# Kernel tuning notes

Measured on AMD Instinct MI355X. Metric: run time of the kernel, lower is better.

Reference implementation:

```python
import jax, jax.numpy as jnp
import numpy as np

V, E, H, T, B, D, L = 32000, 512, 512, 128, 4, 4, 2
C0, C1 = 2000, 10000          # adaptive softmax cutoffs
NT = T - D + 1


def setup_inputs() -> dict:
    key = jax.random.key(0)
    ks = jax.random.split(key, 18)
    s = 0.02
    x = jax.random.randint(ks[0], (B, T), 1, V)
    lengths = jnp.sort(jax.random.randint(ks[1], (B,), D, T + 1))[::-1]
    lengths = lengths.at[0].set(T)
    # graph predictor output: per-layer attention matrices [B, L, T, T]
    G = jax.nn.softmax(jax.random.normal(ks[2], (B, L, T, T)), axis=-1)
    emb = (jax.random.normal(ks[3], (V, E)) * s).at[0].set(0.0)  # padding_idx=0
    enc_w_ih = jax.random.normal(ks[4], (L, 3 * H, H)) * s
    enc_w_hh = jax.random.normal(ks[5], (L, 3 * H, H)) * s
    enc_b_ih = jnp.zeros((L, 3 * H))
    enc_b_hh = jnp.zeros((L, 3 * H))
    dec_w_ih = jax.random.normal(ks[6], (3 * H, E)) * s
    dec_w_hh = jax.random.normal(ks[7], (3 * H, H)) * s
    dec_b_ih = jnp.zeros((3 * H,))
    dec_b_hh = jnp.zeros((3 * H,))
    head_w = jax.random.normal(ks[8], (C0 + 2, H)) * s
    t0_proj = jax.random.normal(ks[9], (H // 4, H)) * s
    t0_out = jax.random.normal(ks[10], (C1 - C0, H // 4)) * s
    t1_proj = jax.random.normal(ks[11], (H // 16, H)) * s
    t1_out = jax.random.normal(ks[12], (V - C1, H // 16)) * s
    return dict(x=x, lengths=lengths, G=G, emb=emb,
                enc_w_ih=enc_w_ih, enc_w_hh=enc_w_hh, enc_b_ih=enc_b_ih, enc_b_hh=enc_b_hh,
                dec_w_ih=dec_w_ih, dec_w_hh=dec_w_hh, dec_b_ih=dec_b_ih, dec_b_hh=dec_b_hh,
                head_w=head_w, t0_proj=t0_proj, t0_out=t0_out, t1_proj=t1_proj, t1_out=t1_out)


def gru_step(xt, h, w_ih, w_hh, b_ih, b_hh):
    """torch nn.GRU/GRUCell math; works on arbitrary leading dims."""
    gi = xt @ w_ih.T + b_ih
    gh = h @ w_hh.T + b_hh
    i_r, i_z, i_n = jnp.split(gi, 3, axis=-1)
    h_r, h_z, h_n = jnp.split(gh, 3, axis=-1)
    r = jax.nn.sigmoid(i_r + h_r)
    z = jax.nn.sigmoid(i_z + h_z)
    n = jnp.tanh(i_n + r * h_n)
    return (1.0 - z) * n + z * h


def adaptive_log_prob(h, head_w, t0_proj, t0_out, t1_proj, t1_out):
    """torch AdaptiveLogSoftmaxWithLoss.log_prob: h [N,H] -> [N,V]."""
    head_lp = jax.nn.log_softmax(h @ head_w.T, axis=-1)                      # [N, C0+2]
    lp0 = head_lp[:, C0:C0 + 1] + jax.nn.log_softmax((h @ t0_proj.T) @ t0_out.T, axis=-1)
    lp1 = head_lp[:, C0 + 1:C0 + 2] + jax.nn.log_softmax((h @ t1_proj.T) @ t1_out.T, axis=-1)
    return jnp.concatenate([head_lp[:, :C0], lp0, lp1], axis=-1)


def reference(x, lengths, G, emb, enc_w_ih, enc_w_hh, enc_b_ih, enc_b_hh,
              dec_w_ih, dec_w_hh, dec_b_ih, dec_b_hh,
              head_w, t0_proj, t0_out, t1_proj, t1_out):
    b = x.shape[0]
    input_f = emb[x]                      # [B,T,E] (dropout p=0)
    embedded = input_f
    # ---- encoder: graph-weighted aggregation + GRUCell per layer ----
    for l in range(enc_w_ih.shape[0]):
        wgt = jnp.einsum('bji,bjd->bid', G[:, l], input_f)   # G_l^T @ input_f
        input_f = gru_step(wgt, input_f, enc_w_ih[l], enc_w_hh[l], enc_b_ih[l], enc_b_hh[l])
    # ---- decoder: length-D GRU window per start position t ----
    t_idx = jnp.arange(NT)
    d_idx = jnp.arange(D)
    tok_idx = jnp.broadcast_to(t_idx[None, :, None] + d_idx[None, None, :] - 1, (b, NT, D))
    tok_idx = tok_idx.at[:, 0, 0].set(lengths - 1)           # t=0,d=0 uses embedded[lengths-1]
    wins = jnp.take_along_axis(embedded, tok_idx.reshape(b, -1)[:, :, None], axis=1)
    wins = wins.reshape(b, NT, D, E)
    h0 = input_f[:, :NT, :]                                  # [B,NT,H]
    def step(h, xd):
        hn = gru_step(xd, h, dec_w_ih, dec_w_hh, dec_b_ih, dec_b_hh)
        return hn, hn
    _, hs = jax.lax.scan(step, h0, jnp.moveaxis(wins, 2, 0))  # [D,B,NT,H]
    hs = jnp.moveaxis(hs, 0, 2)                               # [B,NT,D,H]
    # pad_packed_sequence zeros hidden beyond per-row lens = min(lengths - t, D)
    valid = (t_idx[None, :, None] + d_idx[None, None, :]) < lengths[:, None, None]
    hs = jnp.where(valid[..., None], hs, 0.0)
    lp = adaptive_log_prob(hs.reshape(-1, H), head_w, t0_proj, t0_out, t1_proj, t1_out)
    lp = lp.reshape(b, NT, D, V)
    # batch rows with lengths <= t were excluded and F.pad'ed with zeros
    row_valid = t_idx[None, :] < lengths[:, None]
    lp = jnp.where(row_valid[:, :, None, None], lp, 0.0)
    return lp.reshape(b, NT * D, V)
```

## Files before the change

kernel.cpp:

```cpp
#include <hip/hip_runtime.h>
#include <hip/hip_bf16.h>

typedef __hip_bfloat16 bf16;
typedef __attribute__((ext_vector_type(8))) short short8v;
typedef __attribute__((ext_vector_type(4))) float float4v;

#define V_    32000
#define E_    512
#define H_    512
#define T_    128
#define B_    4
#define D_    4
#define L_    2
#define C0_   2000
#define C1_   10000
#define NT_   125
#define NROW_ 2000
#define NH_   2002
#define NTOTC 2162
#define NSLOT 252

__device__ __forceinline__ float bf2f(bf16 v) { return __bfloat162float(v); }
__device__ __forceinline__ unsigned short f2bfu(float f) {
    bf16 h = __float2bfloat16(f);
    union { bf16 h; unsigned short u; } cv; cv.h = h; return cv.u;
}
__device__ __forceinline__ float ld1(const void* p, size_t i, int bf) {
    return bf ? bf2f(((const bf16*)p)[i]) : ((const float*)p)[i];
}
__device__ __forceinline__ void st1(void* p, size_t i, int bf, float v) {
    if (bf) ((unsigned short*)p)[i] = f2bfu(v);
    else    ((float*)p)[i] = v;
}

__device__ __forceinline__ void lse_push(float z, float& m, float& s) {
    if (z <= m) { s += __expf(z - m); }
    else        { s = s * __expf(m - z) + 1.0f; m = z; }
}
__device__ __forceinline__ void lse_merge(float m2, float s2, float& m, float& s) {
    float mm = fmaxf(m, m2);
    s = s * __expf(m - mm) + s2 * __expf(m2 - mm);
    m = mm;
}

__global__ void k_detect(const void* __restrict__ G, int* __restrict__ flag) {
    int t = threadIdx.x;
    float s32 = 0.0f;
    for (int k = t; k < 128; k += 64) s32 += ((const float*)G)[k];
    for (int off = 32; off; off >>= 1) s32 += __shfl_down(s32, off);
    if (t == 0) {
        float e32 = fabsf(s32 - 1.0f);
        *flag = (e32 < 0.05f) ? 0 : 1;
    }
}

struct ConvArgs {
    const void* src[9];
    unsigned int off[10];
};
__global__ void k_wconv(ConvArgs a, unsigned short* __restrict__ wb,
                        const int* __restrict__ flagp) {
    const int bf = *flagp;
    unsigned int total = a.off[9];
    for (unsigned int i = blockIdx.x * 256 + threadIdx.x; i < total;
         i += gridDim.x * 256) {
        int seg = 0;
        while (i >= a.off[seg + 1]) seg++;
        wb[i] = f2bfu(ld1(a.src[seg], i - a.off[seg], bf));
    }
}

__global__ void k_embed(const int* __restrict__ x, const void* __restrict__ emb,
                        float* __restrict__ embedded, float* __restrict__ f0,
                        unsigned short* __restrict__ f0b,
                        const int* __restrict__ flagp) {
    const int bf = *flagp;
    int i = blockIdx.x * 256 + threadIdx.x;
    int bt = i >> 9, e = i & 511;
    int tok = x[bt];
    float v = ld1(emb, (size_t)tok * E_ + e, bf);
    embedded[i] = v; f0[i] = v; f0b[i] = f2bfu(v);
}

__global__ void k_wgt(const void* __restrict__ G, const float* __restrict__ f,
                      unsigned short* __restrict__ wgtb, int l,
                      const int* __restrict__ flagp) {
    const int bf = *flagp;
    int i = blockIdx.x * 256 + threadIdx.x;
    int e = i & 511;
    int bi = i >> 9;
    int b = bi >> 7, ip = bi & 127;
    size_t gbase = ((size_t)(b * L_ + l) * T_ * T_) + ip;
    const float* fb = f + (size_t)b * T_ * E_ + e;
    float acc = 0.0f;
    #pragma unroll 4
    for (int j = 0; j < T_; ++j)
        acc = fmaf(ld1(G, gbase + (size_t)j * T_, bf), fb[(size_t)j * E_], acc);
    wgtb[i] = f2bfu(acc);
}

struct GemmP {
    const unsigned short* A0;
    const unsigned short* A1;
    const unsigned short* W;
    unsigned long long w1off;
    int M, N, K, Nlse;
    float* Zg; int ldz; int zcol1;
    const void* bias0; const void* bias1; int boff;
    void* out; int outColOff;
    float* stats;
    unsigned short* p0b;
    unsigned short* p1b;
    float* lsep; int slotBase;
    const float* corr;
    const int* lengths;
    const int* flagp;
};

template<int MODE>
__global__ void k_gemm(GemmP p) {
    const int bf = *p.flagp;
    const int zsel = blockIdx.z;
    const unsigned short* A  = zsel ? p.A1 : p.A0;
    const unsigned short* Bw = p.W + (zsel ? p.w1off : 0ull);
    const int M = p.M, N = p.N, K = p.K;
    const int bx = blockIdx.x, by = blockIdx.y;
    const int m0 = by * 128, n0 = bx * 128;
    const int t = threadIdx.x;
    const int wave = t >> 6, lane = t & 63;
    const int wm = wave >> 1, wn = wave & 1;
    const int quad = lane >> 4, l16 = lane & 15;

    __shared__ __align__(16) unsigned short As[128 * 40];
    __shared__ __align__(16) unsigned short Bs[128 * 40];
    __shared__ float pm[128][2], ps[128][2];

    float4v acc[4][4];
    #pragma unroll
    for (int mi = 0; mi < 4; ++mi)
        #pragma unroll
        for (int ni = 0; ni < 4; ++ni)
            acc[mi][ni] = (float4v){0.f, 0.f, 0.f, 0.f};

    for (int k0 = 0; k0 < K; k0 += 32) {
        if (k0) __syncthreads();
        #pragma unroll
        for (int i = 0; i < 2; ++i) {
            int idx = t + i * 256;
            int row = idx >> 2, seg = idx & 3;
            uint4 av = {0u, 0u, 0u, 0u};
            int gm = m0 + row;
            if (gm < M) av = *(const uint4*)(A + (size_t)gm * K + k0 + seg * 8);
            *(uint4*)(&As[row * 40 + seg * 8]) = av;
            uint4 bv = {0u, 0u, 0u, 0u};
            int gn = n0 + row;
            if (gn < N) bv = *(const uint4*)(Bw + (size_t)gn * K + k0 + seg * 8);
            *(uint4*)(&Bs[row * 40 + seg * 8]) = bv;
        }
        __syncthreads();
        short8v af[4], bfv[4];
        #pragma unroll
        for (int mi = 0; mi < 4; ++mi)
            af[mi] = *(const short8v*)(As + (wm * 64 + mi * 16 + l16) * 40 + quad * 8);
        #pragma unroll
        for (int ni = 0; ni < 4; ++ni)
            bfv[ni] = *(const short8v*)(Bs + (wn * 64 + ni * 16 + l16) * 40 + quad * 8);
        #pragma unroll
        for (int mi = 0; mi < 4; ++mi)
            #pragma unroll
            for (int ni = 0; ni < 4; ++ni)
                acc[mi][ni] = __builtin_amdgcn_mfma_f32_16x16x32_bf16(
                    af[mi], bfv[ni], acc[mi][ni], 0, 0, 0);
    }

    if (MODE == 0) {
        const void* bias = zsel ? p.bias1 : p.bias0;
        const int zcol = zsel ? p.zcol1 : 0;
        #pragma unroll
        for (int mi = 0; mi < 4; ++mi)
            #pragma unroll
            for (int r = 0; r < 4; ++r) {
                int grow = m0 + wm * 64 + mi * 16 + quad * 4 + r;
                if (grow >= M) continue;
                #pragma unroll
                for (int ni = 0; ni < 4; ++ni) {
                    int gcol = n0 + wn * 64 + ni * 16 + l16;
                    if (gcol < N)
                        p.Zg[(size_t)grow * p.ldz + zcol + gcol] =
                            acc[mi][ni][r] + ld1(bias, p.boff + gcol, bf);
                }
            }
    } else if (MODE == 1) {
        #pragma unroll
        for (int mi = 0; mi < 4; ++mi)
            #pragma unroll
            for (int r = 0; r < 4; ++r) {
                int grow = m0 + wm * 64 + mi * 16 + quad * 4 + r;
                if (grow >= M) continue;
                #pragma unroll
                for (int ni = 0; ni < 4; ++ni) {
                    int gcol = n0 + wn * 64 + ni * 16 + l16;
                    float v = acc[mi][ni][r];
                    if (gcol >= C0_ && gcol < NH_) p.stats[grow * 8 + 2 + (gcol - C0_)] = v;
                    else if (gcol >= NH_ && gcol < 2130) p.p0b[grow * 128 + (gcol - NH_)] = f2bfu(v);
                    else if (gcol >= 2130 && gcol < NTOTC) p.p1b[grow * 32 + (gcol - 2130)] = f2bfu(v);
                }
            }
    } else if (MODE >= 3) {
        const int crIdx = MODE - 3;
        #pragma unroll
        for (int mi = 0; mi < 4; ++mi)
            #pragma unroll
            for (int r = 0; r < 4; ++r) {
                int grow = m0 + wm * 64 + mi * 16 + quad * 4 + r;
                if (grow >= M) continue;
                int b = grow / 500;
                int tt = (grow - b * 500) >> 2;
                bool valid = tt < p.lengths[b];
                float cr = p.corr[grow * 4 + crIdx];
                #pragma unroll
                for (int ni = 0; ni < 4; ++ni) {
                    int gcol = n0 + wn * 64 + ni * 16 + l16;
                    if (gcol < N) {
                        float v = valid ? (acc[mi][ni][r] - cr) : 0.0f;
                        st1(p.out, (size_t)grow * V_ + p.outColOff + gcol, bf, v);
                    }
                }
            }
    }

    if (MODE == 1 || MODE == 2) {
        const int Nlse = p.Nlse;
        #pragma unroll
        for (int mi = 0; mi < 4; ++mi) {
            #pragma unroll
            for (int r = 0; r < 4; ++r) {
                float m = -1e30f, s = 0.0f;
                #pragma unroll
                for (int ni = 0; ni < 4; ++ni) {
                    int gcol = n0 + wn * 64 + ni * 16 + l16;
                    if (gcol < Nlse) lse_push(acc[mi][ni][r], m, s);
                }
                #pragma unroll
                for (int off = 1; off < 16; off <<= 1) {
                    float m2 = __shfl_xor(m, off), s2 = __shfl_xor(s, off);
                    lse_merge(m2, s2, m, s);
                }
                if (l16 == 0) {
                    int rl = wm * 64 + mi * 16 + quad * 4 + r;
                    pm[rl][wn] = m; ps[rl][wn] = s;
                }
            }
        }
        __syncthreads();
        if (t < 128) {
            int grow = m0 + t;
            if (grow < M) {
                float m = pm[t][0], s = ps[t][0];
                lse_merge(pm[t][1], ps[t][1], m, s);
                float* dst = p.lsep + ((size_t)grow * NSLOT + p.slotBase + bx) * 2;
                dst[0] = m; dst[1] = s;
            }
        }
    }
}

__device__ __forceinline__ float gru2(float i_r, float i_z, float i_n,
                                      float h_r, float h_z, float h_n, float h) {
    float r = 1.0f / (1.0f + __expf(-(i_r + h_r)));
    float z = 1.0f / (1.0f + __expf(-(i_z + h_z)));
    float n = tanhf(i_n + r * h_n);
    return (1.0f - z) * n + z * h;
}

__global__ void k_apply_enc(const float* __restrict__ gates,
                            const float* __restrict__ hprev,
                            float* __restrict__ hnext,
                            unsigned short* __restrict__ hnextb) {
    int i = blockIdx.x * 256 + threadIdx.x;
    int row = i >> 9, k = i & 511;
    const float* g = gates + (size_t)row * 3072;
    float v = gru2(g[k], g[512 + k], g[1024 + k],
                   g[1536 + k], g[2048 + k], g[2560 + k], hprev[i]);
    hnext[i] = v; hnextb[i] = f2bfu(v);
}

__global__ void k_h0(const float* __restrict__ ffin, float* __restrict__ hdec,
                     unsigned short* __restrict__ hdecb) {
    int i = blockIdx.x * 256 + threadIdx.x;
    int row = i >> 9, e = i & 511;
    int b = row / NT_, t = row - b * NT_;
    float v = ffin[((size_t)(b * T_ + t) << 9) + e];
    hdec[i] = v; hdecb[i] = f2bfu(v);
}

__global__ void k_winall(const float* __restrict__ embedded,
                         const int* __restrict__ lengths,
                         unsigned short* __restrict__ winb) {
    int i = blockIdx.x * 256 + threadIdx.x;
    int e = i & 511;
    int wr = i >> 9;
    int d = wr / 500, row = wr - d * 500;
    int b = row / NT_, t = row - b * NT_;
    int tok = (d == 0 && t == 0) ? (lengths[b] - 1) : (t + d - 1);
    winb[i] = f2bfu(embedded[((size_t)(b * T_ + tok) << 9) + e]);
}

__global__ void k_apply_dec(const float* __restrict__ gih,
                            const float* __restrict__ ghh,
                            float* __restrict__ hdec,
                            unsigned short* __restrict__ hdecb,
                            unsigned short* __restrict__ hsb,
                            const int* __restrict__ lengths, int d) {
    int i = blockIdx.x * 256 + threadIdx.x;
    int row = i >> 9, k = i & 511;
    int b = row / NT_, t = row - b * NT_;
    const float* gi = gih + (size_t)(d * 500 + row) * 1536;
    const float* gh = ghh + (size_t)row * 1536;
    float hn = gru2(gi[k], gi[512 + k], gi[1024 + k],
                    gh[k], gh[512 + k], gh[1024 + k], hdec[i]);
    hdec[i] = hn; hdecb[i] = f2bfu(hn);
    bool valid = (t + d) < lengths[b];
    hsb[(((size_t)row * D_ + d) << 9) + k] = valid ? f2bfu(hn) : (unsigned short)0;
}

__global__ void k_corr2(const float* __restrict__ lsep, const float* __restrict__ stats,
                        float* __restrict__ corr) {
    int r = blockIdx.x * 256 + threadIdx.x;
    if (r >= NROW_) return;
    const float* P = lsep + (size_t)r * NSLOT * 2;
    float m = -1e30f, s = 0.0f;
    for (int i = 0; i < 17; ++i)  lse_merge(P[2 * i], P[2 * i + 1], m, s);
    float ch = m + logf(s);
    float lp0 = stats[r * 8 + 2] - ch;
    float lp1 = stats[r * 8 + 3] - ch;
    m = -1e30f; s = 0.0f;
    for (int i = 17; i < 80; ++i) lse_merge(P[2 * i], P[2 * i + 1], m, s);
    float ct0 = m + logf(s);
    m = -1e30f; s = 0.0f;
    for (int i = 80; i < 252; ++i) lse_merge(P[2 * i], P[2 * i + 1], m, s);
    float ct1 = m + logf(s);
    corr[r * 4 + 0] = ch;
    corr[r * 4 + 1] = ct0 - lp0;
    corr[r * 4 + 2] = ct1 - lp1;
}

#define OFF_EMB    0u
#define OFF_FA     262144u
#define OFF_FB     524288u
#define OFF_FAB    786432u
#define OFF_FBB    917504u
#define OFF_WGTB   1048576u
#define OFF_GATES  1179648u
#define OFF_GIH    2752512u
#define OFF_GHH    5824512u
#define OFF_HDEC   6592512u
#define OFF_HDECB  6848512u
#define OFF_WINB   6976512u
#define OFF_HSB    7488512u
#define OFF_P0B    8000512u
#define OFF_P1B    8128512u
#define OFF_STATS  8160512u
#define OFF_CORR   8176512u
#define OFF_LSEP   8184512u
#define OFF_WB     9192512u
#define OFF_FLAG   12969264u

#define WO_ENCIH   0u
#define WO_ENCHH   1572864u
#define WO_DECIH   3145728u
#define WO_DECHH   3932160u
#define WO_W1      4718592u
#define WO_T0O     5825536u
#define WO_T1O     6849536u
#define WO_END     7553504u

static inline GemmP mkp(const unsigned short* A0, const unsigned short* A1,
                        const unsigned short* W, unsigned long long w1off,
                        int M, int N, int K, int Nlse,
                        float* Zg, int ldz, int zcol1,
                        const void* bias0, const void* bias1, int boff,
                        void* out, int outColOff, float* stats,
                        unsigned short* p0b, unsigned short* p1b,
                        float* lsep, int slotBase, const float* corr,
                        const int* lengths, const int* flagp) {
    GemmP p;
    p.A0 = A0; p.A1 = A1; p.W = W; p.w1off = w1off;
    p.M = M; p.N = N; p.K = K; p.Nlse = Nlse;
    p.Zg = Zg; p.ldz = ldz; p.zcol1 = zcol1;
    p.bias0 = bias0; p.bias1 = bias1; p.boff = boff;
    p.out = out; p.outColOff = outColOff; p.stats = stats;
    p.p0b = p0b; p.p1b = p1b; p.lsep = lsep; p.slotBase = slotBase;
    p.corr = corr; p.lengths = lengths; p.flagp = flagp;
    return p;
}

extern "C" void kernel_launch(void* const* d_in, const int* in_sizes, int n_in,
                              void* d_out, int out_size, void* d_ws, size_t ws_size,
                              hipStream_t stream) {
    (void)in_sizes; (void)n_in; (void)out_size; (void)ws_size;
    const int*  x        = (const int*)d_in[0];
    const int*  lengths  = (const int*)d_in[1];
    const void* G        = d_in[2];
    const void* emb      = d_in[3];
    const void* enc_w_ih = d_in[4];
    const void* enc_w_hh = d_in[5];
    const void* enc_b_ih = d_in[6];
    const void* enc_b_hh = d_in[7];
    const void* dec_w_ih = d_in[8];
    const void* dec_w_hh = d_in[9];
    const void* dec_b_ih = d_in[10];
    const void* dec_b_hh = d_in[11];
    const void* head_w   = d_in[12];
    const void* t0_proj  = d_in[13];
    const void* t0_out   = d_in[14];
    const void* t1_proj  = d_in[15];
    const void* t1_out   = d_in[16];

    float* ws = (float*)d_ws;
    float* embedded = ws + OFF_EMB;
    float* fA    = ws + OFF_FA;
    float* fB    = ws + OFF_FB;
    unsigned short* fAb  = (unsigned short*)(ws + OFF_FAB);
    unsigned short* fBb  = (unsigned short*)(ws + OFF_FBB);
    unsigned short* wgtb = (unsigned short*)(ws + OFF_WGTB);
    float* gates = ws + OFF_GATES;
    float* gih   = ws + OFF_GIH;
    float* ghh   = ws + OFF_GHH;
    float* hdec  = ws + OFF_HDEC;
    unsigned short* hdecb = (unsigned short*)(ws + OFF_HDECB);
    unsigned short* winb  = (unsigned short*)(ws + OFF_WINB);
    unsigned short* hsb   = (unsigned short*)(ws + OFF_HSB);
    unsigned short* p0b   = (unsigned short*)(ws + OFF_P0B);
    unsigned short* p1b   = (unsigned short*)(ws + OFF_P1B);
    float* stats = ws + OFF_STATS;
    float* corr  = ws + OFF_CORR;
    float* lsep  = ws + OFF_LSEP;
    unsigned short* WB = (unsigned short*)(ws + OFF_WB);
    int* flagp = (int*)(ws + OFF_FLAG);
    void* out = d_out;

    k_detect<<<1, 64, 0, stream>>>(G, flagp);

    ConvArgs ca;
    ca.src[0] = enc_w_ih; ca.src[1] = enc_w_hh; ca.src[2] = dec_w_ih;
    ca.src[3] = dec_w_hh; ca.src[4] = head_w;   ca.src[5] = t0_proj;
    ca.src[6] = t1_proj;  ca.src[7] = t0_out;   ca.src[8] = t1_out;
    ca.off[0] = WO_ENCIH; ca.off[1] = WO_ENCHH; ca.off[2] = WO_DECIH;
    ca.off[3] = WO_DECHH; ca.off[4] = WO_W1;
    ca.off[5] = WO_W1 + 2002u * 512u;
    ca.off[6] = WO_W1 + 2130u * 512u;
    ca.off[7] = WO_T0O;   ca.off[8] = WO_T1O;   ca.off[9] = WO_END;
    k_wconv<<<4096, 256, 0, stream>>>(ca, WB, flagp);

    k_embed<<<1024, 256, 0, stream>>>(x, emb, embedded, fA, fAb, flagp);

    k_wgt<<<1024, 256, 0, stream>>>(G, fA, wgtb, 0, flagp);
    k_gemm<0><<<dim3(12, 4, 2), 256, 0, stream>>>(mkp(
        wgtb, fAb, WB + WO_ENCIH, (unsigned long long)(WO_ENCHH - WO_ENCIH),
        512, 1536, 512, 0, gates, 3072, 1536, enc_b_ih, enc_b_hh, 0,
        nullptr, 0, nullptr, nullptr, nullptr, nullptr, 0, nullptr, lengths, flagp));
    k_apply_enc<<<1024, 256, 0, stream>>>(gates, fA, fB, fBb);

    k_wgt<<<1024, 256, 0, stream>>>(G, fB, wgtb, 1, flagp);
    k_gemm<0><<<dim3(12, 4, 2), 256, 0, stream>>>(mkp(
        wgtb, fBb, WB + WO_ENCIH + 786432u, (unsigned long long)(WO_ENCHH - WO_ENCIH),
        512, 1536, 512, 0, gates, 3072, 1536, enc_b_ih, enc_b_hh, 1536,
        nullptr, 0, nullptr, nullptr, nullptr, nullptr, 0, nullptr, lengths, flagp));
    k_apply_enc<<<1024, 256, 0, stream>>>(gates, fB, fA, fAb);

    k_h0<<<1000, 256, 0, stream>>>(fA, hdec, hdecb);
    k_winall<<<4000, 256, 0, stream>>>(embedded, lengths, winb);
    k_gemm<0><<<dim3(12, 16, 1), 256, 0, stream>>>(mkp(
        winb, nullptr, WB + WO_DECIH, 0ull, 2000, 1536, 512, 0,
        gih, 1536, 0, dec_b_ih, nullptr, 0,
        nullptr, 0, nullptr, nullptr, nullptr, nullptr, 0, nullptr, lengths, flagp));
    for (int d = 0; d < D_; ++d) {
        k_gemm<0><<<dim3(12, 4, 1), 256, 0, stream>>>(mkp(
            hdecb, nullptr, WB + WO_DECHH, 0ull, 500, 1536, 512, 0,
            ghh, 1536, 0, dec_b_hh, nullptr, 0,
            nullptr, 0, nullptr, nullptr, nullptr, nullptr, 0, nullptr, lengths, flagp));
        k_apply_dec<<<1000, 256, 0, stream>>>(gih, ghh, hdec, hdecb, hsb, lengths, d);
    }

    k_gemm<1><<<dim3(17, 16, 1), 256, 0, stream>>>(mkp(
        hsb, nullptr, WB + WO_W1, 0ull, NROW_, NTOTC, 512, NH_,
        nullptr, 0, 0, nullptr, nullptr, 0, nullptr, 0,
        stats, p0b, p1b, lsep, 0, nullptr, lengths, flagp));
    k_gemm<2><<<dim3(63, 16, 1), 256, 0, stream>>>(mkp(
        p0b, nullptr, WB + WO_T0O, 0ull, NROW_, 8000, 128, 8000,
        nullptr, 0, 0, nullptr, nullptr, 0, nullptr, 0,
        stats, nullptr, nullptr, lsep, 17, nullptr, lengths, flagp));
    k_gemm<2><<<dim3(172, 16, 1), 256, 0, stream>>>(mkp(
        p1b, nullptr, WB + WO_T1O, 0ull, NROW_, 22000, 32, 22000,
        nullptr, 0, 0, nullptr, nullptr, 0, nullptr, 0,
        stats, nullptr, nullptr, lsep, 80, nullptr, lengths, flagp));

    k_corr2<<<8, 256, 0, stream>>>(lsep, stats, corr);

    k_gemm<3><<<dim3(16, 16, 1), 256, 0, stream>>>(mkp(
        hsb, nullptr, WB + WO_W1, 0ull, NROW_, C0_, 512, 0,
        nullptr, 0, 0, nullptr, nullptr, 0, out, 0,
        nullptr, nullptr, nullptr, nullptr, 0, corr, lengths, flagp));
    k_gemm<4><<<dim3(63, 16, 1), 256, 0, stream>>>(mkp(
        p0b, nullptr, WB + WO_T0O, 0ull, NROW_, 8000, 128, 0,
        nullptr, 0, 0, nullptr, nullptr, 0, out, C0_,
        nullptr, nullptr, nullptr, nullptr, 0, corr, lengths, flagp));
    k_gemm<5><<<dim3(172, 16, 1), 256, 0, stream>>>(mkp(
        p1b, nullptr, WB + WO_T1O, 0ull, NROW_, 22000, 32, 0,
        nullptr, 0, 0, nullptr, nullptr, 0, out, C1_,
        nullptr, nullptr, nullptr, nullptr, 0, corr, lengths, flagp));
}
```

Measured before the change: 801.5 us.

## Merge adaptive-softmax GEMM launches, split-K decoder GEMM, fuse setup kernels

Merges the weight conversion and embedding lookup into one launch, and the h0 copy and window gather into another. The tail-cluster log-sum-exp GEMMs and the three output GEMMs each become a single launch that dispatches on blockIdx. The wide tail1 GEMM processes four N-tiles per block to amortise the tiny K=32 prologue. The small recurrent decoder GEMM is split four ways along K, with partial sums written to separate buffers, and the workspace layout is enlarged to hold them. The intent is fewer launches and better occupancy. The cost is extra partial-sum traffic and a gate kernel that must now reduce the slices.

```diff
diff --git a/kernel.cpp b/kernel.cpp
--- a/kernel.cpp
+++ b/kernel.cpp
@@ -1,5 +1,6 @@
 #include <hip/hip_runtime.h>
 #include <hip/hip_bf16.h>
+#include <cstring>
 
 typedef __hip_bfloat16 bf16;
 typedef __attribute__((ext_vector_type(8))) short short8v;
@@ -58,28 +59,28 @@
     const void* src[9];
     unsigned int off[10];
 };
-__global__ void k_wconv(ConvArgs a, unsigned short* __restrict__ wb,
-                        const int* __restrict__ flagp) {
+__global__ void k_wembed(ConvArgs a, unsigned short* __restrict__ wb,
+                         const int* __restrict__ flagp,
+                         const int* __restrict__ x, const void* __restrict__ emb,
+                         float* __restrict__ embedded, float* __restrict__ f0,
+                         unsigned short* __restrict__ f0b) {
     const int bf = *flagp;
-    unsigned int total = a.off[9];
-    for (unsigned int i = blockIdx.x * 256 + threadIdx.x; i < total;
-         i += gridDim.x * 256) {
-        int seg = 0;
-        while (i >= a.off[seg + 1]) seg++;
-        wb[i] = f2bfu(ld1(a.src[seg], i - a.off[seg], bf));
-    }
-}
-
-__global__ void k_embed(const int* __restrict__ x, const void* __restrict__ emb,
-                        float* __restrict__ embedded, float* __restrict__ f0,
-                        unsigned short* __restrict__ f0b,
-                        const int* __restrict__ flagp) {
-    const int bf = *flagp;
-    int i = blockIdx.x * 256 + threadIdx.x;
-    int bt = i >> 9, e = i & 511;
-    int tok = x[bt];
-    float v = ld1(emb, (size_t)tok * E_ + e, bf);
-    embedded[i] = v; f0[i] = v; f0b[i] = f2bfu(v);
+    if (blockIdx.x < 1024) {
+        int i = blockIdx.x * 256 + threadIdx.x;
+        int bt = i >> 9, e = i & 511;
+        int tok = x[bt];
+        float v = ld1(emb, (size_t)tok * E_ + e, bf);
+        embedded[i] = v; f0[i] = v; f0b[i] = f2bfu(v);
+    } else {
+        unsigned int total = a.off[9];
+        unsigned int stride = (gridDim.x - 1024) * 256;
+        for (unsigned int i = (blockIdx.x - 1024) * 256 + threadIdx.x; i < total;
+             i += stride) {
+            int seg = 0;
+            while (i >= a.off[seg + 1]) seg++;
+            wb[i] = f2bfu(ld1(a.src[seg], i - a.off[seg], bf));
+        }
+    }
 }
 
 __global__ void k_wgt(const void* __restrict__ G, const float* __restrict__ f,
@@ -115,154 +116,199 @@
     const float* corr;
     const int* lengths;
     const int* flagp;
+    int gx;
+    int nrep;
+    int crIdx;
+    int ksplit;
 };
 
 template<int MODE>
-__global__ void k_gemm(GemmP p) {
+__device__ __forceinline__ void gemm_core(const GemmP& p, int bx, int by,
+        unsigned short* As, unsigned short* Bs,
+        float (*pm)[2], float (*ps)[2]) {
     const int bf = *p.flagp;
-    const int zsel = blockIdx.z;
+    int zsel = 0, kslice = 0;
+    if (MODE == 0) {
+        if (p.ksplit > 1) kslice = blockIdx.z;
+        else              zsel   = blockIdx.z;
+    }
     const unsigned short* A  = zsel ? p.A1 : p.A0;
     const unsigned short* Bw = p.W + (zsel ? p.w1off : 0ull);
     const int M = p.M, N = p.N, K = p.K;
-    const int bx = blockIdx.x, by = blockIdx.y;
-    const int m0 = by * 128, n0 = bx * 128;
+    const int m0 = by * 128;
     const int t = threadIdx.x;
     const int wave = t >> 6, lane = t & 63;
     const int wm = wave >> 1, wn = wave & 1;
     const int quad = lane >> 4, l16 = lane & 15;
-
+    const int kcnt = K / p.ksplit;
+    const int kbeg = kslice * kcnt;
+
+    for (int nr = 0; nr < p.nrep; ++nr) {
+        const int ntile = bx * p.nrep + nr;
+        const int n0 = ntile * 128;
+
+        float4v acc[4][4];
+        #pragma unroll
+        for (int mi = 0; mi < 4; ++mi)
+            #pragma unroll
+            for (int ni = 0; ni < 4; ++ni)
+                acc[mi][ni] = (float4v){0.f, 0.f, 0.f, 0.f};
+
+        for (int kk = 0; kk < kcnt; kk += 32) {
+            const int k0 = kbeg + kk;
+            if (kk | nr) __syncthreads();
+            #pragma unroll
+            for (int i = 0; i < 2; ++i) {
+                int idx = t + i * 256;
+                int row = idx >> 2, seg = idx & 3;
+                uint4 av = {0u, 0u, 0u, 0u};
+                int gm = m0 + row;
+                if (gm < M) av = *(const uint4*)(A + (size_t)gm * K + k0 + seg * 8);
+                *(uint4*)(&As[row * 40 + seg * 8]) = av;
+                uint4 bv = {0u, 0u, 0u, 0u};
+                int gn = n0 + row;
+                if (gn < N) bv = *(const uint4*)(Bw + (size_t)gn * K + k0 + seg * 8);
+                *(uint4*)(&Bs[row * 40 + seg * 8]) = bv;
+            }
+            __syncthreads();
+            short8v af[4], bfv[4];
+            #pragma unroll
+            for (int mi = 0; mi < 4; ++mi)
+                af[mi] = *(const short8v*)(As + (wm * 64 + mi * 16 + l16) * 40 + quad * 8);
+            #pragma unroll
+            for (int ni = 0; ni < 4; ++ni)
+                bfv[ni] = *(const short8v*)(Bs + (wn * 64 + ni * 16 + l16) * 40 + quad * 8);
+            #pragma unroll
+            for (int mi = 0; mi < 4; ++mi)
+                #pragma unroll
+                for (int ni = 0; ni < 4; ++ni)
+                    acc[mi][ni] = __builtin_amdgcn_mfma_f32_16x16x32_bf16(
+                        af[mi], bfv[ni], acc[mi][ni], 0, 0, 0);
+        }
+
+        if (MODE == 0) {
+            const void* bias = zsel ? p.bias1 : p.bias0;
+            const int zcol = zsel ? p.zcol1 : 0;
+            float* Z = p.Zg + (size_t)kslice * p.M * p.ldz;
+            #pragma unroll
+            for (int mi = 0; mi < 4; ++mi)
+                #pragma unroll
+                for (int r = 0; r < 4; ++r) {
+                    int grow = m0 + wm * 64 + mi * 16 + quad * 4 + r;
+                    if (grow >= M) continue;
+                    #pragma unroll
+                    for (int ni = 0; ni < 4; ++ni) {
+                        int gcol = n0 + wn * 64 + ni * 16 + l16;
+                        if (gcol < N) {
+                            float bv = (kslice == 0) ? ld1(bias, p.boff + gcol, bf) : 0.0f;
+                            Z[(size_t)grow * p.ldz + zcol + gcol] = acc[mi][ni][r] + bv;
+                        }
+                    }
+                }
+        } else if (MODE == 1) {
+            #pragma unroll
+            for (int mi = 0; mi < 4; ++mi)
+                #pragma unroll
+                for (int r = 0; r < 4; ++r) {
+                    int grow = m0 + wm * 64 + mi * 16 + quad * 4 + r;
+                    if (grow >= M) continue;
+                    #pragma unroll
+                    for (int ni = 0; ni < 4; ++ni) {
+                        int gcol = n0 + wn * 64 + ni * 16 + l16;
+                        float v = acc[mi][ni][r];
+                        if (gcol >= C0_ && gcol < NH_) p.stats[grow * 8 + 2 + (gcol - C0_)] = v;
+                        else if (gcol >= NH_ && gcol < 2130) p.p0b[grow * 128 + (gcol - NH_)] = f2bfu(v);
+                        else if (gcol >= 2130 && gcol < NTOTC) p.p1b[grow * 32 + (gcol - 2130)] = f2bfu(v);
+                    }
+                }
+        } else if (MODE == 3) {
+            const int crIdx = p.crIdx;
+            #pragma unroll
+            for (int mi = 0; mi < 4; ++mi)
+                #pragma unroll
+                for (int r = 0; r < 4; ++r) {
+                    int grow = m0 + wm * 64 + mi * 16 + quad * 4 + r;
+                    if (grow >= M) continue;
+                    int b = grow / 500;
+                    int tt = (grow - b * 500) >> 2;
+                    bool valid = tt < p.lengths[b];
+                    float cr = p.corr[grow * 4 + crIdx];
+                    #pragma unroll
+                    for (int ni = 0; ni < 4; ++ni) {
+                        int gcol = n0 + wn * 64 + ni * 16 + l16;
+                        if (gcol < N) {
+                            float v = valid ? (acc[mi][ni][r] - cr) : 0.0f;
+                            st1(p.out, (size_t)grow * V_ + p.outColOff + gcol, bf, v);
+                        }
+                    }
+                }
+        }
+
+        if (MODE == 1 || MODE == 2) {
+            const int Nlse = p.Nlse;
+            #pragma unroll
+            for (int mi = 0; mi < 4; ++mi) {
+                #pragma unroll
+                for (int r = 0; r < 4; ++r) {
+                    float m = -1e30f, s = 0.0f;
+                    #pragma unroll
+                    for (int ni = 0; ni < 4; ++ni) {
+                        int gcol = n0 + wn * 64 + ni * 16 + l16;
+                        if (gcol < Nlse) lse_push(acc[mi][ni][r], m, s);
+                    }
+                    #pragma unroll
+                    for (int off = 1; off < 16; off <<= 1) {
+                        float m2 = __shfl_xor(m, off), s2 = __shfl_xor(s, off);
+                        lse_merge(m2, s2, m, s);
+                    }
+                    if (l16 == 0) {
+                        int rl = wm * 64 + mi * 16 + quad * 4 + r;
+                        pm[rl][wn] = m; ps[rl][wn] = s;
+                    }
+                }
+            }
+            __syncthreads();
+            if (t < 128) {
+                int grow = m0 + t;
+                if (grow < M) {
+                    float m = pm[t][0], s = ps[t][0];
+                    lse_merge(pm[t][1], ps[t][1], m, s);
+                    float* dst = p.lsep + ((size_t)grow * NSLOT + p.slotBase + ntile) * 2;
+                    dst[0] = m; dst[1] = s;
+                }
+            }
+        }
+    }
+}
+
+__global__ void k_gemm0(GemmP p) {
     __shared__ __align__(16) unsigned short As[128 * 40];
     __shared__ __align__(16) unsigned short Bs[128 * 40];
     __shared__ float pm[128][2], ps[128][2];
-
-    float4v acc[4][4];
-    #pragma unroll
-    for (int mi = 0; mi < 4; ++mi)
-        #pragma unroll
-        for (int ni = 0; ni < 4; ++ni)
-            acc[mi][ni] = (float4v){0.f, 0.f, 0.f, 0.f};
-
-    for (int k0 = 0; k0 < K; k0 += 32) {
-        if (k0) __syncthreads();
-        #pragma unroll
-        for (int i = 0; i < 2; ++i) {
-            int idx = t + i * 256;
-            int row = idx >> 2, seg = idx & 3;
-            uint4 av = {0u, 0u, 0u, 0u};
-            int gm = m0 + row;
-            if (gm < M) av = *(const uint4*)(A + (size_t)gm * K + k0 + seg * 8);
-            *(uint4*)(&As[row * 40 + seg * 8]) = av;
-            uint4 bv = {0u, 0u, 0u, 0u};
-            int gn = n0 + row;
-            if (gn < N) bv = *(const uint4*)(Bw + (size_t)gn * K + k0 + seg * 8);
-            *(uint4*)(&Bs[row * 40 + seg * 8]) = bv;
-        }
-        __syncthreads();
-        short8v af[4], bfv[4];
-        #pragma unroll
-        for (int mi = 0; mi < 4; ++mi)
-            af[mi] = *(const short8v*)(As + (wm * 64 + mi * 16 + l16) * 40 + quad * 8);
-        #pragma unroll
-        for (int ni = 0; ni < 4; ++ni)
-            bfv[ni] = *(const short8v*)(Bs + (wn * 64 + ni * 16 + l16) * 40 + quad * 8);
-        #pragma unroll
-        for (int mi = 0; mi < 4; ++mi)
-            #pragma unroll
-            for (int ni = 0; ni < 4; ++ni)
-                acc[mi][ni] = __builtin_amdgcn_mfma_f32_16x16x32_bf16(
-                    af[mi], bfv[ni], acc[mi][ni], 0, 0, 0);
-    }
-
-    if (MODE == 0) {
-        const void* bias = zsel ? p.bias1 : p.bias0;
-        const int zcol = zsel ? p.zcol1 : 0;
-        #pragma unroll
-        for (int mi = 0; mi < 4; ++mi)
-            #pragma unroll
-            for (int r = 0; r < 4; ++r) {
-                int grow = m0 + wm * 64 + mi * 16 + quad * 4 + r;
-                if (grow >= M) continue;
-                #pragma unroll
-                for (int ni = 0; ni < 4; ++ni) {
-                    int gcol = n0 + wn * 64 + ni * 16 + l16;
-                    if (gcol < N)
-                        p.Zg[(size_t)grow * p.ldz + zcol + gcol] =
-                            acc[mi][ni][r] + ld1(bias, p.boff + gcol, bf);
-                }
-            }
-    } else if (MODE == 1) {
-        #pragma unroll
-        for (int mi = 0; mi < 4; ++mi)
-            #pragma unroll
-            for (int r = 0; r < 4; ++r) {
-                int grow = m0 + wm * 64 + mi * 16 + quad * 4 + r;
-                if (grow >= M) continue;
-                #pragma unroll
-                for (int ni = 0; ni < 4; ++ni) {
-                    int gcol = n0 + wn * 64 + ni * 16 + l16;
-                    float v = acc[mi][ni][r];
-                    if (gcol >= C0_ && gcol < NH_) p.stats[grow * 8 + 2 + (gcol - C0_)] = v;
-                    else if (gcol >= NH_ && gcol < 2130) p.p0b[grow * 128 + (gcol - NH_)] = f2bfu(v);
-                    else if (gcol >= 2130 && gcol < NTOTC) p.p1b[grow * 32 + (gcol - 2130)] = f2bfu(v);
-                }
-            }
-    } else if (MODE >= 3) {
-        const int crIdx = MODE - 3;
-        #pragma unroll
-        for (int mi = 0; mi < 4; ++mi)
-            #pragma unroll
-            for (int r = 0; r < 4; ++r) {
-                int grow = m0 + wm * 64 + mi * 16 + quad * 4 + r;
-                if (grow >= M) continue;
-                int b = grow / 500;
-                int tt = (grow - b * 500) >> 2;
-                bool valid = tt < p.lengths[b];
-                float cr = p.corr[grow * 4 + crIdx];
-                #pragma unroll
-                for (int ni = 0; ni < 4; ++ni) {
-                    int gcol = n0 + wn * 64 + ni * 16 + l16;
-                    if (gcol < N) {
-                        float v = valid ? (acc[mi][ni][r] - cr) : 0.0f;
-                        st1(p.out, (size_t)grow * V_ + p.outColOff + gcol, bf, v);
-                    }
-                }
-            }
-    }
-
-    if (MODE == 1 || MODE == 2) {
-        const int Nlse = p.Nlse;
-        #pragma unroll
-        for (int mi = 0; mi < 4; ++mi) {
-            #pragma unroll
-            for (int r = 0; r < 4; ++r) {
-                float m = -1e30f, s = 0.0f;
-                #pragma unroll
-                for (int ni = 0; ni < 4; ++ni) {
-                    int gcol = n0 + wn * 64 + ni * 16 + l16;
-                    if (gcol < Nlse) lse_push(acc[mi][ni][r], m, s);
-                }
-                #pragma unroll
-                for (int off = 1; off < 16; off <<= 1) {
-                    float m2 = __shfl_xor(m, off), s2 = __shfl_xor(s, off);
-                    lse_merge(m2, s2, m, s);
-                }
-                if (l16 == 0) {
-                    int rl = wm * 64 + mi * 16 + quad * 4 + r;
-                    pm[rl][wn] = m; ps[rl][wn] = s;
-                }
-            }
-        }
-        __syncthreads();
-        if (t < 128) {
-            int grow = m0 + t;
-            if (grow < M) {
-                float m = pm[t][0], s = ps[t][0];
-                lse_merge(pm[t][1], ps[t][1], m, s);
-                float* dst = p.lsep + ((size_t)grow * NSLOT + p.slotBase + bx) * 2;
-                dst[0] = m; dst[1] = s;
-            }
-        }
-    }
+    gemm_core<0>(p, blockIdx.x, blockIdx.y, As, Bs, pm, ps);
+}
+__global__ void k_gemm1(GemmP p) {
+    __shared__ __align__(16) unsigned short As[128 * 40];
+    __shared__ __align__(16) unsigned short Bs[128 * 40];
+    __shared__ float pm[128][2], ps[128][2];
+    gemm_core<1>(p, blockIdx.x, blockIdx.y, As, Bs, pm, ps);
+}
+__global__ void k_gemmA2(GemmP pa, GemmP pb) {
+    __shared__ __align__(16) unsigned short As[128 * 40];
+    __shared__ __align__(16) unsigned short Bs[128 * 40];
+    __shared__ float pm[128][2], ps[128][2];
+    int bx = blockIdx.x;
+    if (bx < pa.gx) gemm_core<2>(pa, bx, blockIdx.y, As, Bs, pm, ps);
+    else            gemm_core<2>(pb, bx - pa.gx, blockIdx.y, As, Bs, pm, ps);
+}
+__global__ void k_gemmB3(GemmP pa, GemmP pb, GemmP pc) {
+    __shared__ __align__(16) unsigned short As[128 * 40];
+    __shared__ __align__(16) unsigned short Bs[128 * 40];
+    __shared__ float pm[128][2], ps[128][2];
+    int bx = blockIdx.x;
+    if (bx < pa.gx)              gemm_core<3>(pa, bx, blockIdx.y, As, Bs, pm, ps);
+    else if (bx < pa.gx + pb.gx) gemm_core<3>(pb, bx - pa.gx, blockIdx.y, As, Bs, pm, ps);
+    else                         gemm_core<3>(pc, bx - pa.gx - pb.gx, blockIdx.y, As, Bs, pm, ps);
 }
 
 __device__ __forceinline__ float gru2(float i_r, float i_z, float i_n,
@@ -285,25 +331,27 @@
     hnext[i] = v; hnextb[i] = f2bfu(v);
 }
 
-__global__ void k_h0(const float* __restrict__ ffin, float* __restrict__ hdec,
-                     unsigned short* __restrict__ hdecb) {
+__global__ void k_h0win(const float* __restrict__ embedded,
+                        const float* __restrict__ ffin,
+                        const int* __restrict__ lengths,
+                        unsigned short* __restrict__ winb,
+                        float* __restrict__ hdec,
+                        unsigned short* __restrict__ hdecb) {
     int i = blockIdx.x * 256 + threadIdx.x;
-    int row = i >> 9, e = i & 511;
-    int b = row / NT_, t = row - b * NT_;
-    float v = ffin[((size_t)(b * T_ + t) << 9) + e];
-    hdec[i] = v; hdecb[i] = f2bfu(v);
-}
-
-__global__ void k_winall(const float* __restrict__ embedded,
-                         const int* __restrict__ lengths,
-                         unsigned short* __restrict__ winb) {
-    int i = blockIdx.x * 256 + threadIdx.x;
-    int e = i & 511;
-    int wr = i >> 9;
-    int d = wr / 500, row = wr - d * 500;
-    int b = row / NT_, t = row - b * NT_;
-    int tok = (d == 0 && t == 0) ? (lengths[b] - 1) : (t + d - 1);
-    winb[i] = f2bfu(embedded[((size_t)(b * T_ + tok) << 9) + e]);
+    if (i < 1024000) {
+        int e = i & 511;
+        int wr = i >> 9;
+        int d = wr / 500, row = wr - d * 500;
+        int b = row / NT_, t = row - b * NT_;
+        int tok = (d == 0 && t == 0) ? (lengths[b] - 1) : (t + d - 1);
+        winb[i] = f2bfu(embedded[((size_t)(b * T_ + tok) << 9) + e]);
+    } else {
+        int j = i - 1024000;
+        int row = j >> 9, e = j & 511;
+        int b = row / NT_, t = row - b * NT_;
+        float v = ffin[((size_t)(b * T_ + t) << 9) + e];
+        hdec[j] = v; hdecb[j] = f2bfu(v);
+    }
 }
 
 __global__ void k_apply_dec(const float* __restrict__ gih,
@@ -317,8 +365,13 @@
     int b = row / NT_, t = row - b * NT_;
     const float* gi = gih + (size_t)(d * 500 + row) * 1536;
     const float* gh = ghh + (size_t)row * 1536;
-    float hn = gru2(gi[k], gi[512 + k], gi[1024 + k],
-                    gh[k], gh[512 + k], gh[1024 + k], hdec[i]);
+    float h_r = 0.f, h_z = 0.f, h_n = 0.f;
+    #pragma unroll
+    for (int s = 0; s < 4; ++s) {
+        const float* g = gh + (size_t)s * 768000;
+        h_r += g[k]; h_z += g[512 + k]; h_n += g[1024 + k];
+    }
+    float hn = gru2(gi[k], gi[512 + k], gi[1024 + k], h_r, h_z, h_n, hdec[i]);
     hdec[i] = hn; hdecb[i] = f2bfu(hn);
     bool valid = (t + d) < lengths[b];
     hsb[(((size_t)row * D_ + d) << 9) + k] = valid ? f2bfu(hn) : (unsigned short)0;
@@ -354,17 +407,17 @@
 #define OFF_GATES  1179648u
 #define OFF_GIH    2752512u
 #define OFF_GHH    5824512u
-#define OFF_HDEC   6592512u
-#define OFF_HDECB  6848512u
-#define OFF_WINB   6976512u
-#define OFF_HSB    7488512u
-#define OFF_P0B    8000512u
-#define OFF_P1B    8128512u
-#define OFF_STATS  8160512u
-#define OFF_CORR   8176512u
-#define OFF_LSEP   8184512u
-#define OFF_WB     9192512u
-#define OFF_FLAG   12969264u
+#define OFF_HDEC   8896512u
+#define OFF_HDECB  9152512u
+#define OFF_WINB   9280512u
+#define OFF_HSB    9792512u
+#define OFF_P0B    10304512u
+#define OFF_P1B    10432512u
+#define OFF_STATS  10464512u
+#define OFF_CORR   10480512u
+#define OFF_LSEP   10488512u
+#define OFF_WB     11496512u
+#define OFF_FLAG   15273264u
 
 #define WO_ENCIH   0u
 #define WO_ENCHH   1572864u
@@ -375,23 +428,11 @@
 #define WO_T1O     6849536u
 #define WO_END     7553504u
 
-static inline GemmP mkp(const unsigned short* A0, const unsigned short* A1,
-                        const unsigned short* W, unsigned long long w1off,
-                        int M, int N, int K, int Nlse,
-                        float* Zg, int ldz, int zcol1,
-                        const void* bias0, const void* bias1, int boff,
-                        void* out, int outColOff, float* stats,
-                        unsigned short* p0b, unsigned short* p1b,
-                        float* lsep, int slotBase, const float* corr,
-                        const int* lengths, const int* flagp) {
+static inline GemmP defp(const int* lengths, const int* flagp) {
     GemmP p;
-    p.A0 = A0; p.A1 = A1; p.W = W; p.w1off = w1off;
-    p.M = M; p.N = N; p.K = K; p.Nlse = Nlse;
-    p.Zg = Zg; p.ldz = ldz; p.zcol1 = zcol1;
-    p.bias0 = bias0; p.bias1 = bias1; p.boff = boff;
-    p.out = out; p.outColOff = outColOff; p.stats = stats;
-    p.p0b = p0b; p.p1b = p1b; p.lsep = lsep; p.slotBase = slotBase;
-    p.corr = corr; p.lengths = lengths; p.flagp = flagp;
+    memset(&p, 0, sizeof(p));
+    p.nrep = 1; p.ksplit = 1;
+    p.lengths = lengths; p.flagp = flagp;
     return p;
 }
 
@@ -451,63 +492,89 @@
     ca.off[5] = WO_W1 + 2002u * 512u;
     ca.off[6] = WO_W1 + 2130u * 512u;
     ca.off[7] = WO_T0O;   ca.off[8] = WO_T1O;   ca.off[9] = WO_END;
-    k_wconv<<<4096, 256, 0, stream>>>(ca, WB, flagp);
-
-    k_embed<<<1024, 256, 0, stream>>>(x, emb, embedded, fA, fAb, flagp);
-
-    k_wgt<<<1024, 256, 0, stream>>>(G, fA, wgtb, 0, flagp);
-    k_gemm<0><<<dim3(12, 4, 2), 256, 0, stream>>>(mkp(
-        wgtb, fAb, WB + WO_ENCIH, (unsigned long long)(WO_ENCHH - WO_ENCIH),
-        512, 1536, 512, 0, gates, 3072, 1536, enc_b_ih, enc_b_hh, 0,
-        nullptr, 0, nullptr, nullptr, nullptr, nullptr, 0, nullptr, lengths, flagp));
-    k_apply_enc<<<1024, 256, 0, stream>>>(gates, fA, fB, fBb);
-
-    k_wgt<<<1024, 256, 0, stream>>>(G, fB, wgtb, 1, flagp);
-    k_gemm<0><<<dim3(12, 4, 2), 256, 0, stream>>>(mkp(
-        wgtb, fBb, WB + WO_ENCIH + 786432u, (unsigned long long)(WO_ENCHH - WO_ENCIH),
-        512, 1536, 512, 0, gates, 3072, 1536, enc_b_ih, enc_b_hh, 1536,
-        nullptr, 0, nullptr, nullptr, nullptr, nullptr, 0, nullptr, lengths, flagp));
-    k_apply_enc<<<1024, 256, 0, stream>>>(gates, fB, fA, fAb);
-
-    k_h0<<<1000, 256, 0, stream>>>(fA, hdec, hdecb);
-    k_winall<<<4000, 256, 0, stream>>>(embedded, lengths, winb);
-    k_gemm<0><<<dim3(12, 16, 1), 256, 0, stream>>>(mkp(
-        winb, nullptr, WB + WO_DECIH, 0ull, 2000, 1536, 512, 0,
-        gih, 1536, 0, dec_b_ih, nullptr, 0,
-        nullptr, 0, nullptr, nullptr, nullptr, nullptr, 0, nullptr, lengths, flagp));
+    k_wembed<<<3072, 256, 0, stream>>>(ca, WB, flagp, x, emb, embedded, fA, fAb);
+
+    {
+        GemmP p = defp(lengths, flagp);
+        p.A0 = wgtb; p.A1 = fAb; p.W = WB + WO_ENCIH;
+        p.w1off = (unsigned long long)(WO_ENCHH - WO_ENCIH);
+        p.M = 512; p.N = 1536; p.K = 512;
+        p.Zg = gates; p.ldz = 3072; p.zcol1 = 1536;
+        p.bias0 = enc_b_ih; p.bias1 = enc_b_hh; p.boff = 0;
+        k_wgt<<<1024, 256, 0, stream>>>(G, fA, wgtb, 0, flagp);
+        k_gemm0<<<dim3(12, 4, 2), 256, 0, stream>>>(p);
+        k_apply_enc<<<1024, 256, 0, stream>>>(gates, fA, fB, fBb);
+    }
+
+    {
+        GemmP p = defp(lengths, flagp);
+        p.A0 = wgtb; p.A1 = fBb; p.W = WB + WO_ENCIH + 786432u;
+        p.w1off = (unsigned long long)(WO_ENCHH - WO_ENCIH);
+        p.M = 512; p.N = 1536; p.K = 512;
+        p.Zg = gates; p.ldz = 3072; p.zcol1 = 1536;
+        p.bias0 = enc_b_ih; p.bias1 = enc_b_hh; p.boff = 1536;
+        k_wgt<<<1024, 256, 0, stream>>>(G, fB, wgtb, 1, flagp);
+        k_gemm0<<<dim3(12, 4, 2), 256, 0, stream>>>(p);
+        k_apply_enc<<<1024, 256, 0, stream>>>(gates, fB, fA, fAb);
+    }
+
+    k_h0win<<<5000, 256, 0, stream>>>(embedded, fA, lengths, winb, hdec, hdecb);
+
+    {
+        GemmP p = defp(lengths, flagp);
+        p.A0 = winb; p.W = WB + WO_DECIH;
+        p.M = 2000; p.N = 1536; p.K = 512;
+        p.Zg = gih; p.ldz = 1536;
+        p.bias0 = dec_b_ih; p.boff = 0;
+        k_gemm0<<<dim3(12, 16, 1), 256, 0, stream>>>(p);
+    }
+
     for (int d = 0; d < D_; ++d) {
-        k_gemm<0><<<dim3(12, 4, 1), 256, 0, stream>>>(mkp(
-            hdecb, nullptr, WB + WO_DECHH, 0ull, 500, 1536, 512, 0,
-            ghh, 1536, 0, dec_b_hh, nullptr, 0,
-            nullptr, 0, nullptr, nullptr, nullptr, nullptr, 0, nullptr, lengths, flagp));
+        GemmP p = defp(lengths, flagp);
+        p.A0 = hdecb; p.W = WB + WO_DECHH;
+        p.M = 500; p.N = 1536; p.K = 512; p.ksplit = 4;
+        p.Zg = ghh; p.ldz = 1536;
+        p.bias0 = dec_b_hh; p.boff = 0;
+        k_gemm0<<<dim3(12, 4, 4), 256, 0, stream>>>(p);
         k_apply_dec<<<1000, 256, 0, stream>>>(gih, ghh, hdec, hdecb, hsb, lengths, d);
     }
 
-    k_gemm<1><<<dim3(17, 16, 1), 256, 0, stream>>>(mkp(
-        hsb, nullptr, WB + WO_W1, 0ull, NROW_, NTOTC, 512, NH_,
-        nullptr, 0, 0, nullptr, nullptr, 0, nullptr, 0,
-        stats, p0b, p1b, lsep, 0, nullptr, lengths, flagp));
-    k_gemm<2><<<dim3(63, 16, 1), 256, 0, stream>>>(mkp(
-        p0b, nullptr, WB + WO_T0O, 0ull, NROW_, 8000, 128, 8000,
-        nullptr, 0, 0, nullptr, nullptr, 0, nullptr, 0,
-        stats, nullptr, nullptr, lsep, 17, nullptr, lengths, flagp));
-    k_gemm<2><<<dim3(172, 16, 1), 256, 0, stream>>>(mkp(
-        p1b, nullptr, WB + WO_T1O, 0ull, NROW_, 22000, 32, 22000,
-        nullptr, 0, 0, nullptr, nullptr, 0, nullptr, 0,
-        stats, nullptr, nullptr, lsep, 80, nullptr, lengths, flagp));
+    {
+        GemmP p = defp(lengths, flagp);
+        p.A0 = hsb; p.W = WB + WO_W1;
+        p.M = NROW_; p.N = NTOTC; p.K = 512; p.Nlse = NH_;
+        p.stats = stats; p.p0b = p0b; p.p1b = p1b;
+        p.lsep = lsep; p.slotBase = 0;
+        k_gemm1<<<dim3(17, 16, 1), 256, 0, stream>>>(p);
+    }
+    {
+        GemmP pa = defp(lengths, flagp);
+        pa.A0 = p0b; pa.W = WB + WO_T0O;
+        pa.M = NROW_; pa.N = 8000; pa.K = 128; pa.Nlse = 8000;
+        pa.lsep = lsep; pa.slotBase = 17; pa.gx = 63;
+        GemmP pb = defp(lengths, flagp);
+        pb.A0 = p1b; pb.W = WB + WO_T1O;
+        pb.M = NROW_; pb.N = 22000; pb.K = 32; pb.Nlse = 22000;
+        pb.lsep = lsep; pb.slotBase = 80; pb.gx = 43; pb.nrep = 4;
+        k_gemmA2<<<dim3(106, 16, 1), 256, 0, stream>>>(pa, pb);
+    }
 
     k_corr2<<<8, 256, 0, stream>>>(lsep, stats, corr);
 
-    k_gemm<3><<<dim3(16, 16, 1), 256, 0, stream>>>(mkp(
-        hsb, nullptr, WB + WO_W1, 0ull, NROW_, C0_, 512, 0,
-        nullptr, 0, 0, nullptr, nullptr, 0, out, 0,
-        nullptr, nullptr, nullptr, nullptr, 0, corr, lengths, flagp));
-    k_gemm<4><<<dim3(63, 16, 1), 256, 0, stream>>>(mkp(
-        p0b, nullptr, WB + WO_T0O, 0ull, NROW_, 8000, 128, 0,
-        nullptr, 0, 0, nullptr, nullptr, 0, out, C0_,
-        nullptr, nullptr, nullptr, nullptr, 0, corr, lengths, flagp));
-    k_gemm<5><<<dim3(172, 16, 1), 256, 0, stream>>>(mkp(
-        p1b, nullptr, WB + WO_T1O, 0ull, NROW_, 22000, 32, 0,
-        nullptr, 0, 0, nullptr, nullptr, 0, out, C1_,
-        nullptr, nullptr, nullptr, nullptr, 0, corr, lengths, flagp));
-}
+    {
+        GemmP pa = defp(lengths, flagp);
+        pa.A0 = hsb; pa.W = WB + WO_W1;
+        pa.M = NROW_; pa.N = C0_; pa.K = 512;
+        pa.out = out; pa.outColOff = 0; pa.corr = corr; pa.crIdx = 0; pa.gx = 16;
+        GemmP pb = defp(lengths, flagp);
+        pb.A0 = p0b; pb.W = WB + WO_T0O;
+        pb.M = NROW_; pb.N = 8000; pb.K = 128;
+        pb.out = out; pb.outColOff = C0_; pb.corr = corr; pb.crIdx = 1; pb.gx = 63;
+        GemmP pc = defp(lengths, flagp);
+        pc.A0 = p1b; pc.W = WB + WO_T1O;
+        pc.M = NROW_; pc.N = 22000; pc.K = 32;
+        pc.out = out; pc.outColOff = C1_; pc.corr = corr; pc.crIdx = 2;
+        pc.gx = 43; pc.nrep = 4;
+        k_gemmB3<<<dim3(122, 16, 1), 256, 0, stream>>>(pa, pb, pc);
+    }
+}
```

Result: slower. 1.029 ms (+28.3%).
